# Performance work log

Hardware: AMD Instinct MI355X
Metric: run time of the kernel (lower is better)

The kernel has to match this reference:

```python
import jax, jax.numpy as jnp
import numpy as np

B, S, D, H, FD = 2, 2048, 1024, 16, 64
DK = D // H
ALPHA = 1.0


def _l2norm(t):
    # matches F.normalize(p=2, dim=-1): divide by max(norm, eps)
    n = jnp.linalg.norm(t, axis=-1, keepdims=True)
    return t / jnp.maximum(n, 1e-12)


def setup_inputs() -> dict:
    key = jax.random.key(0)
    ks = jax.random.split(key, 12)
    sc = 0.02
    return {
        "x": jax.random.normal(ks[0], (B, S, D), jnp.float32),
        "features": jax.random.normal(ks[1], (B, S, FD), jnp.float32),
        "requirements": jax.random.normal(ks[2], (B, S, FD), jnp.float32),
        "Wq": jax.random.normal(ks[3], (D, D), jnp.float32) * sc,
        "bq": jnp.zeros((D,), jnp.float32),
        "Wk": jax.random.normal(ks[4], (D, D), jnp.float32) * sc,
        "bk": jnp.zeros((D,), jnp.float32),
        "Wv": jax.random.normal(ks[5], (D, D), jnp.float32) * sc,
        "bv": jnp.zeros((D,), jnp.float32),
        "Wo": jax.random.normal(ks[6], (D, D), jnp.float32) * sc,
        "bo": jnp.zeros((D,), jnp.float32),
        "pos_ids": jax.random.randint(ks[7], (B, S), 0, 8),
        "causal_mask": jnp.tril(jnp.ones((S, S), bool)),
    }


def reference(x, features, requirements, Wq, bq, Wk, bk, Wv, bv, Wo, bo,
              pos_ids, causal_mask):
    # q/k/v projections -> [B, S, H, DK]
    Q = (x @ Wq + bq).reshape(B, S, H, DK)
    K = (x @ Wk + bk).reshape(B, S, H, DK)
    V = (x @ Wv + bv).reshape(B, S, H, DK)

    # scaled QK^T: [B, H, S, S]
    scores = jnp.einsum('bshd,bthd->bhst', Q, K) / np.sqrt(DK).astype(np.float32)

    # ASA bias (features_only mode): cosine compat req_i . feat_j -> [B, S, S]
    bias = jnp.einsum('bsf,btf->bst', _l2norm(requirements), _l2norm(features))
    scores = scores + ALPHA * bias[:, None, :, :]

    # causal mask (True = allowed)
    scores = jnp.where(causal_mask[None, None, :, :], scores, -jnp.inf)

    weights = jax.nn.softmax(scores, axis=-1)
    weights = jnp.nan_to_num(weights, nan=0.0)

    out = jnp.einsum('bhst,bthd->bshd', weights, V).reshape(B, S, D)
    return out @ Wo + bo
```

## Files before the change

kernel.cpp:

```cpp
#include <hip/hip_runtime.h>
#include <hip/hip_bf16.h>
#include <math.h>

#define Bb 2
#define Ss 2048
#define Dd 1024
#define Hh 16
#define DK 64
#define FD 64

#define LOG2E 1.4426950408889634f

typedef short short8 __attribute__((ext_vector_type(8)));
typedef float f32x4 __attribute__((ext_vector_type(4)));
typedef unsigned int u32;

static __device__ inline ushort f2bf(float f) {
    union { float f; unsigned u; } v; v.f = f;
    unsigned r = v.u + 0x7FFF + ((v.u >> 16) & 1);
    return (ushort)(r >> 16);
}

static __device__ inline uint cvt_pk_bf16(float lo, float hi) {
    uint r;
    asm("v_cvt_pk_bf16_f32 %0, %1, %2" : "=v"(r) : "v"(lo), "v"(hi));
    return r;
}
static __device__ inline float fexp2(float x) {
    return __builtin_amdgcn_exp2f(x);
}

static __device__ inline void gload_lds16(const ushort* g, ushort* l) {
    __builtin_amdgcn_global_load_lds((const __attribute__((address_space(1))) u32*)g,
                                     (__attribute__((address_space(3))) u32*)l, 16, 0, 0);
}

__global__ __launch_bounds__(256) void cast_bf16(const float* __restrict__ in,
                                                 ushort* __restrict__ out) {
    size_t p = (size_t)blockIdx.x * 256 + threadIdx.x;
    float2 v = *(const float2*)(in + 2 * p);
    ((uint*)out)[p] = (uint)f2bf(v.x) | ((uint)f2bf(v.y) << 16);
}

__global__ __launch_bounds__(256) void transpose_cast4(const float* __restrict__ W0,
                                                       const float* __restrict__ W1,
                                                       const float* __restrict__ W2,
                                                       const float* __restrict__ W3,
                                                       ushort* __restrict__ WT) {
    __shared__ float T[64][65];
    const float* W = blockIdx.z == 0 ? W0 : blockIdx.z == 1 ? W1 : blockIdx.z == 2 ? W2 : W3;
    ushort* dst = WT + (size_t)blockIdx.z * Dd * Dd;
    const int k0 = blockIdx.x * 64, n0 = blockIdx.y * 64;
    const int tid = threadIdx.x;
#pragma unroll
    for (int i = 0; i < 4; ++i) {
        int kr = i * 16 + (tid >> 4);
        int nc = (tid & 15) * 4;
        float4 v = *(const float4*)(W + (size_t)(k0 + kr) * Dd + n0 + nc);
        T[kr][nc] = v.x; T[kr][nc + 1] = v.y; T[kr][nc + 2] = v.z; T[kr][nc + 3] = v.w;
    }
    __syncthreads();
    int nr = tid >> 2;
    int kc = (tid & 3) * 16;
    uint pk[8];
#pragma unroll
    for (int j = 0; j < 8; ++j)
        pk[j] = (uint)f2bf(T[kc + 2 * j][nr]) | ((uint)f2bf(T[kc + 2 * j + 1][nr]) << 16);
    uint* o = (uint*)(dst + (size_t)(n0 + nr) * Dd + k0 + kc);
    *(int4*)o = *(int4*)&pk[0];
    *(int4*)(o + 4) = *(int4*)&pk[4];
}

__global__ __launch_bounds__(256) void l2norm2(const float* __restrict__ fsrc,
                                               const float* __restrict__ rsrc,
                                               float* __restrict__ fn,
                                               float* __restrict__ rn) {
    int row = blockIdx.x * 4 + (threadIdx.x >> 6);
    int lane = threadIdx.x & 63;
    const float* in = fsrc; float* out = fn; int r = row;
    if (row >= Bb * Ss) { in = rsrc; out = rn; r = row - Bb * Ss; }
    float v = in[(size_t)r * FD + lane];
    float s = v * v;
#pragma unroll
    for (int off = 32; off; off >>= 1) s += __shfl_xor(s, off, 64);
    out[(size_t)r * FD + lane] = v / fmaxf(sqrtf(s), 1e-12f);
}

__global__ __launch_bounds__(256) void pack_aux(const float* __restrict__ rn,
                                                const float* __restrict__ fn,
                                                ushort* __restrict__ Qext,
                                                ushort* __restrict__ Kext) {
    size_t p = (size_t)blockIdx.x * 256 + threadIdx.x;
    int j = (int)(p & 31);
    size_t row = p >> 5;
    int s = (int)(row & (Ss - 1));
    int bh = (int)(row >> 11);
    int b = bh >> 4;
    size_t src = ((size_t)(b * Ss + s)) * FD + j * 2;
    float2 r2 = *(const float2*)(rn + src);
    float2 f2 = *(const float2*)(fn + src);
    ((uint*)Qext)[row * 64 + 32 + j] =
        (uint)f2bf(r2.x * LOG2E) | ((uint)f2bf(r2.y * LOG2E) << 16);
    ((uint*)Kext)[row * 64 + 32 + j] = (uint)f2bf(f2.x) | ((uint)f2bf(f2.y) << 16);
}

__global__ __launch_bounds__(256) void pack_vt(const ushort* __restrict__ Vrow,
                                               ushort* __restrict__ Vt) {
    __shared__ ushort T[64][72];
    const int tid = threadIdx.x;
    const int s0 = blockIdx.x * 64;
    const int h = blockIdx.y, b = blockIdx.z;
#pragma unroll
    for (int i = 0; i < 2; ++i) {
        int f = tid + i * 256;
        int sr = f >> 3, dc = (f & 7) * 8;
        *(int4*)&T[sr][dc] =
            *(const int4*)(Vrow + ((size_t)((b * Hh + h) * Ss) + s0 + sr) * 64 + dc);
    }
    __syncthreads();
    int d = tid >> 2;
    int sg = (tid & 3) * 16;
    uint pk[8];
#pragma unroll
    for (int j = 0; j < 8; ++j)
        pk[j] = (uint)T[sg + 2 * j][d] | ((uint)T[sg + 2 * j + 1][d] << 16);
    uint* dst = (uint*)(Vt + ((size_t)((b * Hh + h) * DK + d)) * Ss + s0 + sg);
    *(int4*)dst = *(int4*)&pk[0];
    *(int4*)(dst + 4) = *(int4*)&pk[4];
}

__global__ __launch_bounds__(256) void gemm_qkv(const ushort* __restrict__ xb,
                                                const ushort* __restrict__ WT,
                                                const float* __restrict__ bq,
                                                const float* __restrict__ bk,
                                                const float* __restrict__ bv,
                                                ushort* __restrict__ Qext,
                                                ushort* __restrict__ Kext,
                                                ushort* __restrict__ Vrow) {
    __shared__ ushort smem[17408];
    ushort (*As)[64] = (ushort (*)[64])smem;
    ushort (*Bs)[64] = (ushort (*)[64])(smem + 8192);
    const int tid = threadIdx.x;
    const int lane = tid & 63, wave = tid >> 6;
    const int col = lane & 15, quad = lane >> 4;
    const int wm = wave >> 1, wn = wave & 1;
    const int id = blockIdx.x >> 3;
    const int n0 = (blockIdx.x & 7) * 128;
    const int m0 = blockIdx.y * 128;
    const ushort* BTw = WT + (size_t)id * Dd * Dd;
    const float* bias = id == 0 ? bq : id == 1 ? bk : bv;

    const int l8 = lane >> 3;
    const int srcg = (lane & 7) ^ l8;
    const ushort* aS[4]; const ushort* bS[4];
    ushort* aD[4]; ushort* bD[4];
#pragma unroll
    for (int i = 0; i < 4; ++i) {
        int r = wave * 32 + i * 8 + l8;
        aS[i] = xb  + (size_t)(m0 + r) * Dd + srcg * 8;
        bS[i] = BTw + (size_t)(n0 + r) * Dd + srcg * 8;
        aD[i] = smem + (wave * 4 + i) * 512;
        bD[i] = smem + 8192 + (wave * 4 + i) * 512;
    }
    const int xs = col & 7;

    f32x4 acc[4][4] = {};

    for (int k0 = 0; k0 < Dd; k0 += 64) {
        __syncthreads();
#pragma unroll
        for (int i = 0; i < 4; ++i) {
            gload_lds16(aS[i] + k0, aD[i]);
            gload_lds16(bS[i] + k0, bD[i]);
        }
        __syncthreads();
#pragma unroll
        for (int kk = 0; kk < 2; ++kk) {
            short8 af[4], bf[4];
#pragma unroll
            for (int i = 0; i < 4; ++i) {
                af[i] = *(const short8*)&As[wm * 64 + i * 16 + col][((kk * 4 + quad) ^ xs) * 8];
                bf[i] = *(const short8*)&Bs[wn * 64 + i * 16 + col][((kk * 4 + quad) ^ xs) * 8];
            }
#pragma unroll
            for (int i = 0; i < 4; ++i)
#pragma unroll
                for (int j = 0; j < 4; ++j)
                    acc[i][j] = __builtin_amdgcn_mfma_f32_16x16x32_bf16(af[i], bf[j], acc[i][j], 0, 0, 0);
        }
    }

    __syncthreads();
    ushort (*Ep)[136] = (ushort (*)[136])smem;
    const float scl = (id == 0) ? 0.125f * LOG2E : 1.0f;
#pragma unroll
    for (int j = 0; j < 4; ++j) {
        int n_local = wn * 64 + j * 16 + col;
        float bvl = bias[n0 + n_local];
#pragma unroll
        for (int i = 0; i < 4; ++i) {
            int mb = wm * 64 + i * 16 + quad * 4;
#pragma unroll
            for (int reg = 0; reg < 4; ++reg)
                Ep[mb + reg][n_local] = f2bf((acc[i][j][reg] + bvl) * scl);
        }
    }
    __syncthreads();
    {
        const int mrow = tid >> 1;
        const int half = tid & 1;
        const int b = m0 >> 11, s = (m0 & (Ss - 1)) + mrow;
        const int hh = (n0 >> 6) + half;
        if (id == 2) {
            ushort* drow = Vrow + ((size_t)(b * Hh + hh) * Ss + s) * 64;
#pragma unroll
            for (int k = 0; k < 8; ++k)
                *(int4*)(drow + k * 8) = *(int4*)&Ep[mrow][half * 64 + k * 8];
        } else {
            ushort* drow = (id == 0 ? Qext : Kext) + ((size_t)(b * Hh + hh) * Ss + s) * 128;
#pragma unroll
            for (int k = 0; k < 8; ++k)
                *(int4*)(drow + k * 8) = *(int4*)&Ep[mrow][half * 64 + k * 8];
        }
    }
}

__global__ __launch_bounds__(256) void gemm_out(const ushort* __restrict__ Ab,
                                                const ushort* __restrict__ BT,
                                                const float* __restrict__ bias,
                                                float* __restrict__ C) {
    __shared__ ushort As[128][64];
    __shared__ ushort Bs[128][64];
    const int tid = threadIdx.x;
    const int lane = tid & 63, wave = tid >> 6;
    const int col = lane & 15, quad = lane >> 4;
    const int wm = wave >> 1, wn = wave & 1;
    const int n0 = blockIdx.x * 128;
    const int m0 = blockIdx.y * 128;

    const int l8 = lane >> 3;
    const int srcg = (lane & 7) ^ l8;
    const ushort* aS[4]; const ushort* bS[4];
    ushort* aD[4]; ushort* bD[4];
#pragma unroll
    for (int i = 0; i < 4; ++i) {
        int r = wave * 32 + i * 8 + l8;
        aS[i] = Ab + (size_t)(m0 + r) * Dd + srcg * 8;
        bS[i] = BT + (size_t)(n0 + r) * Dd + srcg * 8;
        aD[i] = &As[0][0] + (wave * 4 + i) * 512;
        bD[i] = &Bs[0][0] + (wave * 4 + i) * 512;
    }
    const int xs = col & 7;

    f32x4 acc[4][4] = {};

    for (int k0 = 0; k0 < Dd; k0 += 64) {
        __syncthreads();
#pragma unroll
        for (int i = 0; i < 4; ++i) {
            gload_lds16(aS[i] + k0, aD[i]);
            gload_lds16(bS[i] + k0, bD[i]);
        }
        __syncthreads();
#pragma unroll
        for (int kk = 0; kk < 2; ++kk) {
            short8 af[4], bf[4];
#pragma unroll
            for (int i = 0; i < 4; ++i) {
                af[i] = *(const short8*)&As[wm * 64 + i * 16 + col][((kk * 4 + quad) ^ xs) * 8];
                bf[i] = *(const short8*)&Bs[wn * 64 + i * 16 + col][((kk * 4 + quad) ^ xs) * 8];
            }
#pragma unroll
            for (int i = 0; i < 4; ++i)
#pragma unroll
                for (int j = 0; j < 4; ++j)
                    acc[i][j] = __builtin_amdgcn_mfma_f32_16x16x32_bf16(af[i], bf[j], acc[i][j], 0, 0, 0);
        }
    }

#pragma unroll
    for (int j = 0; j < 4; ++j) {
        int n = n0 + wn * 64 + j * 16 + col;
        float bvl = bias[n];
#pragma unroll
        for (int i = 0; i < 4; ++i) {
#pragma unroll
            for (int reg = 0; reg < 4; ++reg) {
                int m = m0 + wm * 64 + i * 16 + quad * 4 + reg;
                C[(size_t)m * Dd + n] = acc[i][j][reg] + bvl;
            }
        }
    }
}

#define ABQ 128

__global__ __launch_bounds__(512) void attn_mfma12(const ushort* __restrict__ Qe,
                                                   const ushort* __restrict__ Ke,
                                                   const ushort* __restrict__ Vt,
                                                   ushort* __restrict__ Ob) {
    __shared__ ushort Ks[64][128];
    __shared__ ushort Vts[64][64];
    __shared__ ushort PsT[8][16][64];

    const int tid = threadIdx.x;
    const int wave = tid >> 6, lane = tid & 63;
    const int col = lane & 15, quad = lane >> 4;

    const int id = blockIdx.x;
    const int rep = id >> 8;
    const int slot = id & 255;
    const int bh = slot >> 3;
    const int qh = slot & 7;
    const int qt = rep ? qh : (15 - qh);
    const int b = bh >> 4, h = bh & 15;
    const int q0 = qt * ABQ;
    const int rowb = q0 + wave * 16;

    short8 qf[4];
    {
        const ushort* qp = Qe + ((size_t)bh * Ss + rowb + col) * 128 + quad * 8;
#pragma unroll
        for (int k0 = 0; k0 < 4; ++k0) qf[k0] = *(const short8*)(qp + k0 * 32);
    }

    const f32x4 zero4 = {0.f, 0.f, 0.f, 0.f};
    f32x4 oaccT[4] = {zero4, zero4, zero4, zero4};
    float lsum = 0.f;

    const ushort* Kbase = Ke + (size_t)bh * Ss * 128;
    const ushort* Vbase = Vt + (size_t)bh * 64 * Ss;
    const int xsw = col & 7;

    const int Gk0 = wave * 64 + lane;
    const int rk0 = Gk0 >> 4, sk0 = (Gk0 & 15) ^ (rk0 & 7);
    const int Gk1 = 512 + Gk0;
    const int rk1 = Gk1 >> 4, sk1 = (Gk1 & 15) ^ (rk1 & 7);
    const int Gv = Gk0;
    const int rv = Gv >> 3, sv = (Gv & 7) ^ (rv & 7);
    const ushort* ksrc0 = Kbase + (size_t)rk0 * 128 + sk0 * 8;
    const ushort* ksrc1 = Kbase + (size_t)rk1 * 128 + sk1 * 8;
    const ushort* vsrc  = Vbase + (size_t)rv * Ss + sv * 8;
    ushort* kdst0 = &Ks[0][0] + wave * 512;
    ushort* kdst1 = &Ks[0][0] + 4096 + wave * 512;
    ushort* vdst  = &Vts[0][0] + wave * 512;

    const int ntiles = 2 * qt + 2;
    for (int t = 0; t < ntiles; ++t) {
        const int j0 = t * 64;
        __syncthreads();
        gload_lds16(ksrc0, kdst0);   ksrc0 += 64 * 128;
        gload_lds16(ksrc1, kdst1);   ksrc1 += 64 * 128;
        gload_lds16(vsrc,  vdst);    vsrc  += 64;
        __syncthreads();

        if (j0 > rowb + 15) continue;

        f32x4 sacc[4] = {zero4, zero4, zero4, zero4};
        __builtin_amdgcn_s_setprio(1);
#pragma unroll
        for (int c = 0; c < 4; ++c)
#pragma unroll
            for (int k0 = 0; k0 < 4; ++k0) {
                short8 kf = *(const short8*)&Ks[c * 16 + col][((k0 * 4 + quad) ^ xsw) * 8];
                sacc[c] = __builtin_amdgcn_mfma_f32_16x16x32_bf16(kf, qf[k0], sacc[c], 0, 0, 0);
            }
        __builtin_amdgcn_s_setprio(0);

        const bool diag = (j0 + 63 >= rowb);
        if (diag) {
            const int qrow_rel = rowb + col - j0;
#pragma unroll
            for (int c = 0; c < 4; ++c)
#pragma unroll
                for (int reg = 0; reg < 4; ++reg) {
                    float s = sacc[c][reg];
                    if (c * 16 + quad * 4 + reg > qrow_rel) s = -1e9f;
                    float p = fexp2(fminf(s, 28.853901f));
                    lsum += p;
                    sacc[c][reg] = p;
                }
        } else {
#pragma unroll
            for (int c = 0; c < 4; ++c)
#pragma unroll
                for (int reg = 0; reg < 4; ++reg) {
                    float p = fexp2(fminf(sacc[c][reg], 28.853901f));
                    lsum += p;
                    sacc[c][reg] = p;
                }
        }
#pragma unroll
        for (int c = 0; c < 4; ++c) {
            uint2 pk;
            pk.x = cvt_pk_bf16(sacc[c][0], sacc[c][1]);
            pk.y = cvt_pk_bf16(sacc[c][2], sacc[c][3]);
            *(uint2*)&PsT[wave][col][((c * 2 + (quad >> 1)) ^ xsw) * 8 + (quad & 1) * 4] = pk;
        }

        __builtin_amdgcn_s_setprio(1);
#pragma unroll
        for (int k0 = 0; k0 < 2; ++k0) {
            short8 ptf = *(const short8*)&PsT[wave][col][((k0 * 4 + quad) ^ xsw) * 8];
#pragma unroll
            for (int c2 = 0; c2 < 4; ++c2) {
                short8 vtf = *(const short8*)&Vts[c2 * 16 + col][((k0 * 4 + quad) ^ xsw) * 8];
                oaccT[c2] = __builtin_amdgcn_mfma_f32_16x16x32_bf16(vtf, ptf, oaccT[c2], 0, 0, 0);
            }
        }
        __builtin_amdgcn_s_setprio(0);
    }

    {
        float l = lsum;
        l += __shfl_xor(l, 16, 64);
        l += __shfl_xor(l, 32, 64);
        const float inv = 1.f / l;
        ushort* dst = Ob + ((size_t)b * Ss + rowb + col) * Dd + h * DK + quad * 4;
#pragma unroll
        for (int c2 = 0; c2 < 4; ++c2) {
            uint2 pk;
            pk.x = cvt_pk_bf16(oaccT[c2][0] * inv, oaccT[c2][1] * inv);
            pk.y = cvt_pk_bf16(oaccT[c2][2] * inv, oaccT[c2][3] * inv);
            *(uint2*)(dst + c2 * 16) = pk;
        }
    }
}

extern "C" void kernel_launch(void* const* d_in, const int* in_sizes, int n_in,
                              void* d_out, int out_size, void* d_ws, size_t ws_size,
                              hipStream_t stream) {
    const float* x            = (const float*)d_in[0];
    const float* features     = (const float*)d_in[1];
    const float* requirements = (const float*)d_in[2];
    const float* Wq = (const float*)d_in[3];
    const float* bq = (const float*)d_in[4];
    const float* Wk = (const float*)d_in[5];
    const float* bk = (const float*)d_in[6];
    const float* Wv = (const float*)d_in[7];
    const float* bv = (const float*)d_in[8];
    const float* Wo = (const float*)d_in[9];
    const float* bo = (const float*)d_in[10];

    float* out = (float*)d_out;
    float* ws = (float*)d_ws;

    ushort* xb   = (ushort*)(ws);
    ushort* WT   = (ushort*)(ws + 2097152);
    ushort* Qext = (ushort*)(ws + 4194304);
    ushort* Kext = (ushort*)(ws + 8388608);
    ushort* Vrow = (ushort*)(ws + 12582912);
    ushort* Vt   = (ushort*)(ws + 16777216);
    float*  fn   =           ws + 18874368;
    float*  rn   =           ws + 19136512;
    ushort* abb  = (ushort*)(ws + 12582912);

    cast_bf16<<<8192, 256, 0, stream>>>(x, xb);
    transpose_cast4<<<dim3(16, 16, 4), 256, 0, stream>>>(Wq, Wk, Wv, Wo, WT);
    l2norm2<<<2048, 256, 0, stream>>>(features, requirements, fn, rn);
    pack_aux<<<8192, 256, 0, stream>>>(rn, fn, Qext, Kext);

    gemm_qkv<<<dim3(24, 32), 256, 0, stream>>>(xb, WT, bq, bk, bv, Qext, Kext, Vrow);
    pack_vt<<<dim3(Ss / 64, Hh, Bb), 256, 0, stream>>>(Vrow, Vt);

    attn_mfma12<<<dim3(512), 512, 0, stream>>>(Qext, Kext, Vt, abb);

    gemm_out<<<dim3(8, 32), 256, 0, stream>>>(abb, WT + (size_t)3 * Dd * Dd, bo, out);
}
```

Before: 240.0 us.

## Stage 128-key K/V tiles per barrier pair and remap block-to-head order

The attention kernel now loads 128 keys of K and V into LDS per iteration and processes them as two 64-key sub-tiles. This halves the number of __syncthreads pairs and global-to-LDS load rounds. The block index is also remapped so that consecutive blocks cover different heads and interleave heavy and light causal tiles, likely to spread work across XCDs and improve L2 locality. LDS use roughly doubles, which may reduce occupancy, and there is still no double-buffering, so load latency is not overlapped.

Result: slower. 245.5 us (+2.3%).

```diff
diff --git a/kernel.cpp b/kernel.cpp
--- a/kernel.cpp
+++ b/kernel.cpp
@@ -295,12 +295,12 @@
 
 #define ABQ 128
 
-__global__ __launch_bounds__(512) void attn_mfma12(const ushort* __restrict__ Qe,
+__global__ __launch_bounds__(512) void attn_mfma13(const ushort* __restrict__ Qe,
                                                    const ushort* __restrict__ Ke,
                                                    const ushort* __restrict__ Vt,
                                                    ushort* __restrict__ Ob) {
-    __shared__ ushort Ks[64][128];
-    __shared__ ushort Vts[64][64];
+    __shared__ ushort Ks[128][128];
+    __shared__ ushort Vts[64][128];
     __shared__ ushort PsT[8][16][64];
 
     const int tid = threadIdx.x;
@@ -308,10 +308,12 @@
     const int col = lane & 15, quad = lane >> 4;
 
     const int id = blockIdx.x;
-    const int rep = id >> 8;
-    const int slot = id & 255;
-    const int bh = slot >> 3;
-    const int qh = slot & 7;
+    const int x = id & 7;
+    const int k = id >> 3;
+    const int rep = k & 1;
+    const int bhi = (k >> 1) & 3;
+    const int qh = k >> 3;
+    const int bh = bhi * 8 + x;
     const int qt = rep ? qh : (15 - qh);
     const int b = bh >> 4, h = bh & 15;
     const int q0 = qt * ABQ;
@@ -332,83 +334,93 @@
     const ushort* Vbase = Vt + (size_t)bh * 64 * Ss;
     const int xsw = col & 7;
 
-    const int Gk0 = wave * 64 + lane;
-    const int rk0 = Gk0 >> 4, sk0 = (Gk0 & 15) ^ (rk0 & 7);
-    const int Gk1 = 512 + Gk0;
-    const int rk1 = Gk1 >> 4, sk1 = (Gk1 & 15) ^ (rk1 & 7);
-    const int Gv = Gk0;
-    const int rv = Gv >> 3, sv = (Gv & 7) ^ (rv & 7);
-    const ushort* ksrc0 = Kbase + (size_t)rk0 * 128 + sk0 * 8;
-    const ushort* ksrc1 = Kbase + (size_t)rk1 * 128 + sk1 * 8;
-    const ushort* vsrc  = Vbase + (size_t)rv * Ss + sv * 8;
-    ushort* kdst0 = &Ks[0][0] + wave * 512;
-    ushort* kdst1 = &Ks[0][0] + 4096 + wave * 512;
-    ushort* vdst  = &Vts[0][0] + wave * 512;
-
-    const int ntiles = 2 * qt + 2;
-    for (int t = 0; t < ntiles; ++t) {
-        const int j0 = t * 64;
-        __syncthreads();
-        gload_lds16(ksrc0, kdst0);   ksrc0 += 64 * 128;
-        gload_lds16(ksrc1, kdst1);   ksrc1 += 64 * 128;
-        gload_lds16(vsrc,  vdst);    vsrc  += 64;
-        __syncthreads();
-
-        if (j0 > rowb + 15) continue;
-
-        f32x4 sacc[4] = {zero4, zero4, zero4, zero4};
-        __builtin_amdgcn_s_setprio(1);
-#pragma unroll
-        for (int c = 0; c < 4; ++c)
-#pragma unroll
-            for (int k0 = 0; k0 < 4; ++k0) {
-                short8 kf = *(const short8*)&Ks[c * 16 + col][((k0 * 4 + quad) ^ xsw) * 8];
-                sacc[c] = __builtin_amdgcn_mfma_f32_16x16x32_bf16(kf, qf[k0], sacc[c], 0, 0, 0);
-            }
-        __builtin_amdgcn_s_setprio(0);
-
-        const bool diag = (j0 + 63 >= rowb);
-        if (diag) {
-            const int qrow_rel = rowb + col - j0;
+    const ushort* kS[4]; ushort* kD[4];
+#pragma unroll
+    for (int i = 0; i < 4; ++i) {
+        int G = i * 512 + tid;
+        int r = G >> 4, g = G & 15;
+        kS[i] = Kbase + (size_t)r * 128 + (g ^ (r & 7)) * 8;
+        kD[i] = &Ks[0][0] + (i * 512 + wave * 64) * 8;
+    }
+    const ushort* vS[2]; ushort* vD[2];
+#pragma unroll
+    for (int i = 0; i < 2; ++i) {
+        int G = i * 512 + tid;
+        int r = G >> 4, g = G & 15;
+        vS[i] = Vbase + (size_t)r * Ss + (g ^ (r & 7)) * 8;
+        vD[i] = &Vts[0][0] + (i * 512 + wave * 64) * 8;
+    }
+
+    const int nst = qt + 1;
+    for (int t2 = 0; t2 < nst; ++t2) {
+        const int j0b = t2 * 128;
+        const size_t ko = (size_t)j0b * 128;
+        __syncthreads();
+#pragma unroll
+        for (int i = 0; i < 4; ++i) gload_lds16(kS[i] + ko, kD[i]);
+#pragma unroll
+        for (int i = 0; i < 2; ++i) gload_lds16(vS[i] + j0b, vD[i]);
+        __syncthreads();
+
+#pragma unroll
+        for (int sub = 0; sub < 2; ++sub) {
+            const int j0 = j0b + sub * 64;
+            if (j0 > rowb + 15) continue;
+
+            f32x4 sacc[4] = {zero4, zero4, zero4, zero4};
+            __builtin_amdgcn_s_setprio(1);
 #pragma unroll
             for (int c = 0; c < 4; ++c)
 #pragma unroll
-                for (int reg = 0; reg < 4; ++reg) {
-                    float s = sacc[c][reg];
-                    if (c * 16 + quad * 4 + reg > qrow_rel) s = -1e9f;
-                    float p = fexp2(fminf(s, 28.853901f));
-                    lsum += p;
-                    sacc[c][reg] = p;
+                for (int k0 = 0; k0 < 4; ++k0) {
+                    short8 kf = *(const short8*)&Ks[sub * 64 + c * 16 + col][((k0 * 4 + quad) ^ xsw) * 8];
+                    sacc[c] = __builtin_amdgcn_mfma_f32_16x16x32_bf16(kf, qf[k0], sacc[c], 0, 0, 0);
                 }
-        } else {
-#pragma unroll
-            for (int c = 0; c < 4; ++c)
-#pragma unroll
-                for (int reg = 0; reg < 4; ++reg) {
-                    float p = fexp2(fminf(sacc[c][reg], 28.853901f));
-                    lsum += p;
-                    sacc[c][reg] = p;
+            __builtin_amdgcn_s_setprio(0);
+
+            const bool diag = (j0 + 63 >= rowb);
+            if (diag) {
+                const int qrow_rel = rowb + col - j0;
+#pragma unroll
+                for (int c = 0; c < 4; ++c)
+#pragma unroll
+                    for (int reg = 0; reg < 4; ++reg) {
+                        float s = sacc[c][reg];
+                        if (c * 16 + quad * 4 + reg > qrow_rel) s = -1e9f;
+                        float p = fexp2(fminf(s, 28.853901f));
+                        lsum += p;
+                        sacc[c][reg] = p;
+                    }
+            } else {
+#pragma unroll
+                for (int c = 0; c < 4; ++c)
+#pragma unroll
+                    for (int reg = 0; reg < 4; ++reg) {
+                        float p = fexp2(fminf(sacc[c][reg], 28.853901f));
+                        lsum += p;
+                        sacc[c][reg] = p;
+                    }
+            }
+#pragma unroll
+            for (int c = 0; c < 4; ++c) {
+                uint2 pk;
+                pk.x = cvt_pk_bf16(sacc[c][0], sacc[c][1]);
+                pk.y = cvt_pk_bf16(sacc[c][2], sacc[c][3]);
+                *(uint2*)&PsT[wave][col][((c * 2 + (quad >> 1)) ^ xsw) * 8 + (quad & 1) * 4] = pk;
+            }
+
+            __builtin_amdgcn_s_setprio(1);
+#pragma unroll
+            for (int k0 = 0; k0 < 2; ++k0) {
+                short8 ptf = *(const short8*)&PsT[wave][col][((k0 * 4 + quad) ^ xsw) * 8];
+#pragma unroll
+                for (int c2 = 0; c2 < 4; ++c2) {
+                    short8 vtf = *(const short8*)&Vts[c2 * 16 + col][(sub * 8 + ((k0 * 4 + quad) ^ xsw)) * 8];
+                    oaccT[c2] = __builtin_amdgcn_mfma_f32_16x16x32_bf16(vtf, ptf, oaccT[c2], 0, 0, 0);
                 }
-        }
-#pragma unroll
-        for (int c = 0; c < 4; ++c) {
-            uint2 pk;
-            pk.x = cvt_pk_bf16(sacc[c][0], sacc[c][1]);
-            pk.y = cvt_pk_bf16(sacc[c][2], sacc[c][3]);
-            *(uint2*)&PsT[wave][col][((c * 2 + (quad >> 1)) ^ xsw) * 8 + (quad & 1) * 4] = pk;
-        }
-
-        __builtin_amdgcn_s_setprio(1);
-#pragma unroll
-        for (int k0 = 0; k0 < 2; ++k0) {
-            short8 ptf = *(const short8*)&PsT[wave][col][((k0 * 4 + quad) ^ xsw) * 8];
-#pragma unroll
-            for (int c2 = 0; c2 < 4; ++c2) {
-                short8 vtf = *(const short8*)&Vts[c2 * 16 + col][((k0 * 4 + quad) ^ xsw) * 8];
-                oaccT[c2] = __builtin_amdgcn_mfma_f32_16x16x32_bf16(vtf, ptf, oaccT[c2], 0, 0, 0);
-            }
-        }
-        __builtin_amdgcn_s_setprio(0);
+            }
+            __builtin_amdgcn_s_setprio(0);
+        }
     }
 
     {
@@ -463,7 +475,7 @@
     gemm_qkv<<<dim3(24, 32), 256, 0, stream>>>(xb, WT, bq, bk, bv, Qext, Kext, Vrow);
     pack_vt<<<dim3(Ss / 64, Hh, Bb), 256, 0, stream>>>(Vrow, Vt);
 
-    attn_mfma12<<<dim3(512), 512, 0, stream>>>(Qext, Kext, Vt, abb);
+    attn_mfma13<<<dim3(512), 512, 0, stream>>>(Qext, Kext, Vt, abb);
 
     gemm_out<<<dim3(8, 32), 256, 0, stream>>>(abb, WT + (size_t)3 * Dd * Dd, bo, out);
 }
```
